# Kernel optimization log

Measured on AMD Instinct MI355X. Metric: run time of the kernel, lower is better.

The kernel has to match this reference:

```python
import jax, jax.numpy as jnp
import numpy as np
import math

C = 8  # sparsity factor c from __init__


def setup_inputs() -> dict:
    key = jax.random.key(0)
    kq, kk, kv, ki = jax.random.split(key, 4)
    B, Q, KV, D = 4, 2048, 2048, 512
    U = int(Q * math.log(KV))  # 15615 sampled keys, matches torch _sampler
    q = jax.random.normal(kq, (B, Q, D), dtype=jnp.float32)
    k = jax.random.normal(kk, (B, KV, D), dtype=jnp.float32)
    v = jax.random.normal(kv, (B, KV, D), dtype=jnp.float32)
    sample_idx = jax.random.randint(ki, (B, U), 0, KV)  # per-batch random key sample
    return {"q": q, "k": k, "v": v, "sample_idx": sample_idx}


def reference(q, k, v, sample_idx):
    B, Q, D = q.shape
    KV = k.shape[1]
    u = int(C * math.log(Q))  # number of selected queries (== 60 here)

    # _sampler: gather sampled keys per batch -> (B, U, D)
    k_bar = jnp.take_along_axis(k, sample_idx[:, :, None], axis=1)

    # sparsity measure M = max_j s_bar - mean_j s_bar, s_bar: (B, Q, U)
    s_bar = jnp.einsum('bqd,bud->bqu', q, k_bar)
    M = s_bar.max(axis=2) - s_bar.mean(axis=2)  # (B, Q)

    # top-u queries per batch
    _, top_idx = jax.lax.top_k(M, u)  # (B, u)
    q_bar = jnp.take_along_axis(q, top_idx[:, :, None], axis=1)  # (B, u, D)

    # small dense attention over full keys; NOTE: original scales by sqrt(kv_len)
    attn = jnp.einsum('bud,bkd->buk', q_bar, k) / jnp.sqrt(jnp.asarray(KV, q.dtype))
    attn = jax.nn.softmax(attn, axis=-1)
    s1 = jnp.einsum('buk,bkd->bud', attn, v)  # (B, u, D)

    # fill all positions with mean of v, then scatter attention outputs
    s = jnp.broadcast_to(v.mean(axis=1, keepdims=True), q.shape)  # (B, Q, D)
    bidx = jnp.arange(B)[:, None]
    s = s.at[bidx, top_idx].set(s1)
    return s
```

## Files before the change

kernel.cpp:

```cpp
#include <hip/hip_runtime.h>
#include <math.h>

#define BATCH 4
#define QN    2048
#define KVN   2048
#define DN    512
#define U_TOT 15615
#define NSEL  60
#define NSLOT 32
#define S1KS  64

typedef __attribute__((ext_vector_type(8))) short bf16x8;
typedef __attribute__((ext_vector_type(4))) float f32x4;

__device__ __forceinline__ unsigned short f2bf(float f) {
  unsigned u = __float_as_uint(f);
  unsigned r = (u + 0x7fffu + ((u >> 16) & 1u)) >> 16;
  return (unsigned short)r;
}
__device__ __forceinline__ float bf2f(unsigned short h) {
  return __uint_as_float(((unsigned)h) << 16);
}
__device__ __forceinline__ void gld16(const void* g, void* l) {
  __builtin_amdgcn_global_load_lds(
      (const __attribute__((address_space(1))) unsigned int*)g,
      (__attribute__((address_space(3))) unsigned int*)l, 16, 0, 0);
}

__global__ __launch_bounds__(256) void split_kernel(
    const float* __restrict__ q, const float* __restrict__ k,
    unsigned short* __restrict__ qhi, unsigned short* __restrict__ qlo,
    unsigned short* __restrict__ khi, unsigned short* __restrict__ klo)
{
  const int half = blockIdx.x >> 12;
  const int i = (blockIdx.x & 4095) * 256 + threadIdx.x;
  const float* in = half ? k : q;
  unsigned short* hi = half ? khi : qhi;
  unsigned short* lo = half ? klo : qlo;
  float4 f = reinterpret_cast<const float4*>(in)[i];
  ushort4 h, l;
  h.x = f2bf(f.x); l.x = f2bf(f.x - bf2f(h.x));
  h.y = f2bf(f.y); l.y = f2bf(f.y - bf2f(h.y));
  h.z = f2bf(f.z); l.z = f2bf(f.z - bf2f(h.z));
  h.w = f2bf(f.w); l.w = f2bf(f.w - bf2f(h.w));
  reinterpret_cast<ushort4*>(hi)[i] = h;
  reinterpret_cast<ushort4*>(lo)[i] = l;
}

__global__ __launch_bounds__(1024) void count_kernel(
    const int* __restrict__ sidx, float* __restrict__ cnt)
{
  __shared__ int h[KVN];
  const int b = blockIdx.x, t = threadIdx.x;
  for (int i = t; i < KVN; i += 1024) h[i] = 0;
  __syncthreads();
  for (int i = t; i < U_TOT; i += 1024) atomicAdd(&h[sidx[b * U_TOT + i]], 1);
  __syncthreads();
  for (int i = t; i < KVN; i += 1024) cnt[b * KVN + i] = (float)h[i];
}

__global__ __launch_bounds__(256) void s_mfma_kernel(
    const unsigned short* __restrict__ qh, const unsigned short* __restrict__ ql,
    const unsigned short* __restrict__ kh, const unsigned short* __restrict__ kl,
    const float* __restrict__ cnt, float* __restrict__ Pmax, float* __restrict__ Psum)
{
  __shared__ unsigned short Ah[128 * 32];
  __shared__ unsigned short Al[128 * 32];
  __shared__ unsigned short Bh[128 * 32];
  __shared__ unsigned short Bl[128 * 32];
  __shared__ float cnt_s[128];

  const int t = threadIdx.x;
  const int w = t >> 6;
  const int L = t & 63;
  const int mbase = (w & 1) * 64;
  const int nbase = (w >> 1) * 64;
  const int lm = L & 15;

  const int bid = blockIdx.x;
  const int xcd = bid & 7;
  const int idx = bid >> 3;
  const int b   = xcd >> 1;
  const int ji  = (xcd & 1) * 8 + (idx >> 3);
  const int qi0 = (idx & 7) * 2;
  const int j0  = ji * 128;

  if (t < 128) cnt_s[t] = cnt[b * KVN + j0 + t];

  const int srow = t >> 2;
  const int schk = (t & 3) ^ ((t >> 3) & 3);

  const int perm  = (L >> 4) ^ ((lm >> 1) & 3);
  const int abase = (mbase * 4 + lm * 4 + perm) * 8;
  const int bbase = (nbase * 4 + lm * 4 + perm) * 8;

  const size_t koff0 = ((size_t)(b * KVN) + j0 + srow) * DN + (size_t)(schk * 8);
  const size_t koff1 = koff0 + (size_t)64 * DN;

  for (int qq = 0; qq < 2; ++qq) {
    const int q0 = (qi0 + qq) * 128;
    const size_t qoff0 = ((size_t)(b * QN) + q0 + srow) * DN + (size_t)(schk * 8);
    const size_t qoff1 = qoff0 + (size_t)64 * DN;

    f32x4 acc[4][4];
#pragma unroll
    for (int nf = 0; nf < 4; ++nf)
#pragma unroll
      for (int mf = 0; mf < 4; ++mf) {
        acc[nf][mf][0] = 0.f; acc[nf][mf][1] = 0.f;
        acc[nf][mf][2] = 0.f; acc[nf][mf][3] = 0.f;
      }

    for (int d0 = 0; d0 < DN; d0 += 32) {
      __syncthreads();
      gld16(qh + qoff0 + d0, &Ah[t * 8]);
      gld16(qh + qoff1 + d0, &Ah[(t + 256) * 8]);
      gld16(ql + qoff0 + d0, &Al[t * 8]);
      gld16(ql + qoff1 + d0, &Al[(t + 256) * 8]);
      gld16(kh + koff0 + d0, &Bh[t * 8]);
      gld16(kh + koff1 + d0, &Bh[(t + 256) * 8]);
      gld16(kl + koff0 + d0, &Bl[t * 8]);
      gld16(kl + koff1 + d0, &Bl[(t + 256) * 8]);
      __syncthreads();

      bf16x8 ah[4], al[4];
#pragma unroll
      for (int mf = 0; mf < 4; ++mf) {
        ah[mf] = *reinterpret_cast<const bf16x8*>(&Ah[abase + mf * 512]);
        al[mf] = *reinterpret_cast<const bf16x8*>(&Al[abase + mf * 512]);
      }
#pragma unroll
      for (int nf = 0; nf < 4; ++nf) {
        bf16x8 bh = *reinterpret_cast<const bf16x8*>(&Bh[bbase + nf * 512]);
        bf16x8 bl = *reinterpret_cast<const bf16x8*>(&Bl[bbase + nf * 512]);
#pragma unroll
        for (int mf = 0; mf < 4; ++mf) {
          acc[nf][mf] = __builtin_amdgcn_mfma_f32_16x16x32_bf16(ah[mf], bh, acc[nf][mf], 0, 0, 0);
          acc[nf][mf] = __builtin_amdgcn_mfma_f32_16x16x32_bf16(ah[mf], bl, acc[nf][mf], 0, 0, 0);
          acc[nf][mf] = __builtin_amdgcn_mfma_f32_16x16x32_bf16(al[mf], bh, acc[nf][mf], 0, 0, 0);
        }
      }
    }

    float mx[4][4], wsm[4][4];
#pragma unroll
    for (int mf = 0; mf < 4; ++mf)
#pragma unroll
      for (int r = 0; r < 4; ++r) { mx[mf][r] = -INFINITY; wsm[mf][r] = 0.f; }

#pragma unroll
    for (int nf = 0; nf < 4; ++nf) {
      const float c = cnt_s[nbase + nf * 16 + lm];
      const bool has = (c > 0.f);
#pragma unroll
      for (int mf = 0; mf < 4; ++mf)
#pragma unroll
        for (int r = 0; r < 4; ++r) {
          const float v = acc[nf][mf][r];
          if (has) mx[mf][r] = fmaxf(mx[mf][r], v);
          wsm[mf][r] = fmaf(c, v, wsm[mf][r]);
        }
    }

    const size_t spi = (size_t)((ji * 2 + (w >> 1)) * BATCH + b);
#pragma unroll
    for (int mf = 0; mf < 4; ++mf)
#pragma unroll
      for (int r = 0; r < 4; ++r) {
        float m = mx[mf][r], s = wsm[mf][r];
#pragma unroll
        for (int o = 1; o < 16; o <<= 1) {
          m = fmaxf(m, __shfl_xor(m, o));
          s += __shfl_xor(s, o);
        }
        if (lm == 0) {
          const int qrow = q0 + mbase + mf * 16 + (L >> 4) * 4 + r;
          Pmax[spi * QN + qrow] = m;
          Psum[spi * QN + qrow] = s;
        }
      }
  }
}

__global__ __launch_bounds__(256) void combine_kernel(
    const float* __restrict__ Pmax, const float* __restrict__ Psum, float* __restrict__ M)
{
  const int g = blockIdx.x * 256 + threadIdx.x;
  const int b = g >> 11;
  const int qq = g & (QN - 1);
  float m = -INFINITY, s = 0.f;
#pragma unroll 4
  for (int p = 0; p < NSLOT; ++p) {
    m = fmaxf(m, Pmax[((size_t)(p * BATCH + b)) * QN + qq]);
    s += Psum[((size_t)(p * BATCH + b)) * QN + qq];
  }
  M[g] = m - s * (1.0f / (float)U_TOT);
}

__global__ __launch_bounds__(256) void select_kernel(
    const float* __restrict__ M, int* __restrict__ topidx, int* __restrict__ rowslot)
{
  const int b = blockIdx.x;
  const int t = threadIdx.x;
  unsigned long long key[8];
#pragma unroll
  for (int s = 0; s < 8; ++s) {
    const int qq = s * 256 + t;
    unsigned u = __float_as_uint(M[b * QN + qq]);
    u = (u & 0x80000000u) ? ~u : (u | 0x80000000u);
    key[s] = ((unsigned long long)u << 32) | (unsigned)(QN - qq);
    rowslot[b * QN + qq] = -1;
  }

  __shared__ unsigned hist[256];
  __shared__ unsigned long long pref_s;
  __shared__ unsigned rank_s;
  __shared__ unsigned cnt_s;
  if (t == 0) { pref_s = 0ull; rank_s = NSEL; cnt_s = 0u; }
  __syncthreads();

  for (int level = 7; level >= 0; --level) {
    const int shift = level * 8;
    hist[t] = 0;
    __syncthreads();
    const unsigned long long pref = pref_s;
    const unsigned rank = rank_s;
#pragma unroll
    for (int s = 0; s < 8; ++s) {
      const bool match = (level == 7) || ((key[s] >> (shift + 8)) == pref);
      if (match) atomicAdd(&hist[(unsigned)((key[s] >> shift) & 255u)], 1u);
    }
    __syncthreads();
    if (t < 64) {
      const unsigned h0 = hist[4 * t], h1 = hist[4 * t + 1];
      const unsigned h2 = hist[4 * t + 2], h3 = hist[4 * t + 3];
      const unsigned loc = h0 + h1 + h2 + h3;
      unsigned run = loc;
#pragma unroll
      for (int o = 1; o < 64; o <<= 1) {
        const unsigned oth = (unsigned)__shfl_down((int)run, o);
        if (t + o < 64) run += oth;
      }
      const unsigned suf = run - loc;
      const unsigned c3 = suf, c2 = c3 + h3, c1 = c2 + h2, c0 = c1 + h1;
      int hit = -1; unsigned cgt = 0;
      if      (c3 < rank && rank <= c3 + h3) { hit = 4 * t + 3; cgt = c3; }
      else if (c2 < rank && rank <= c2 + h2) { hit = 4 * t + 2; cgt = c2; }
      else if (c1 < rank && rank <= c1 + h1) { hit = 4 * t + 1; cgt = c1; }
      else if (c0 < rank && rank <= c0 + h0) { hit = 4 * t + 0; cgt = c0; }
      if (hit >= 0) {
        pref_s = ((level == 7) ? 0ull : (pref_s << 8)) | (unsigned long long)(unsigned)hit;
        rank_s = rank - cgt;
      }
    }
    __syncthreads();
  }

  const unsigned long long T = pref_s;
#pragma unroll
  for (int s = 0; s < 8; ++s) {
    if (key[s] >= T) {
      const unsigned pos = atomicAdd(&cnt_s, 1u);
      const int qsel = QN - (int)(key[s] & 0xFFFFFFFFull);
      topidx[b * 64 + pos] = qsel;
      rowslot[b * QN + qsel] = (int)pos;
    }
  }
}

#define SBM 64
#define SBN 32
#define SBK 32
__global__ __launch_bounds__(256) void scores_kernel(
    const float* __restrict__ q, const int* __restrict__ topidx,
    const float* __restrict__ k, float* __restrict__ attn)
{
  __shared__ float a_s[SBK][SBM + 4];
  __shared__ float b_s[SBK][SBN + 4];
  __shared__ int tix_s[64];
  const int t  = threadIdx.x;
  const int tx = t & 7;
  const int ty = t >> 3;
  const int kv0 = blockIdx.x * SBN;
  const int b   = blockIdx.y;
  const float* kb = k + (size_t)b * KVN * DN;

  if (t < 64) tix_s[t] = (t < NSEL) ? topidx[b * 64 + t] : 0;
  __syncthreads();

  float acc[2][4];
#pragma unroll
  for (int i = 0; i < 2; ++i)
#pragma unroll
    for (int j = 0; j < 4; ++j) acc[i][j] = 0.f;

  const int c4 = (t & 7) * 4;
  const int r0 = t >> 3;
  const int srow0 = tix_s[r0];
  const int srow1 = tix_s[r0 + 32];

  for (int d0 = 0; d0 < DN; d0 += SBK) {
#pragma unroll
    for (int rr = 0; rr < 2; ++rr) {
      int row = r0 + rr * 32;
      int srow = rr ? srow1 : srow0;
      float4 av = *reinterpret_cast<const float4*>(q + ((size_t)(b * QN) + srow) * DN + d0 + c4);
      a_s[c4 + 0][row] = av.x; a_s[c4 + 1][row] = av.y;
      a_s[c4 + 2][row] = av.z; a_s[c4 + 3][row] = av.w;
    }
    {
      float4 bv = *reinterpret_cast<const float4*>(kb + (size_t)(kv0 + r0) * DN + d0 + c4);
      b_s[c4 + 0][r0] = bv.x; b_s[c4 + 1][r0] = bv.y;
      b_s[c4 + 2][r0] = bv.z; b_s[c4 + 3][r0] = bv.w;
    }
    __syncthreads();
#pragma unroll
    for (int kk = 0; kk < SBK; ++kk) {
      const float a0 = a_s[kk][ty * 2];
      const float a1 = a_s[kk][ty * 2 + 1];
      float4 bv = *reinterpret_cast<const float4*>(&b_s[kk][tx * 4]);
      float bf[4] = {bv.x, bv.y, bv.z, bv.w};
#pragma unroll
      for (int j = 0; j < 4; ++j) {
        acc[0][j] = fmaf(a0, bf[j], acc[0][j]);
        acc[1][j] = fmaf(a1, bf[j], acc[1][j]);
      }
    }
    __syncthreads();
  }

#pragma unroll
  for (int i = 0; i < 2; ++i) {
    int j = ty * 2 + i;
    if (j < NSEL) {
      float4 o = make_float4(acc[i][0], acc[i][1], acc[i][2], acc[i][3]);
      *reinterpret_cast<float4*>(attn + ((size_t)(b * NSEL + j)) * KVN + kv0 + tx * 4) = o;
    }
  }
}

__global__ __launch_bounds__(256) void softmax_kernel(float* __restrict__ attn)
{
  __shared__ float buf[KVN];
  __shared__ float red[256];
  const int t = threadIdx.x;
  float* row = attn + (size_t)blockIdx.x * KVN;

  float m = -INFINITY;
  for (int i = t; i < KVN; i += 256) { float v = row[i]; buf[i] = v; m = fmaxf(m, v); }
  red[t] = m;
  __syncthreads();
  for (int off = 128; off > 0; off >>= 1) {
    if (t < off) red[t] = fmaxf(red[t], red[t + off]);
    __syncthreads();
  }
  m = red[0];
  __syncthreads();

  const float sc = 0.022097086912079608f;
  float s = 0.f;
  for (int i = t; i < KVN; i += 256) { float e = __expf((buf[i] - m) * sc); buf[i] = e; s += e; }
  red[t] = s;
  __syncthreads();
  for (int off = 128; off > 0; off >>= 1) {
    if (t < off) red[t] += red[t + off];
    __syncthreads();
  }
  float inv = 1.f / red[0];
  for (int i = t; i < KVN; i += 256) row[i] = buf[i] * inv;
}

__global__ __launch_bounds__(256) void s1_partial_kernel(
    const float* __restrict__ attn, const float* __restrict__ v,
    float* __restrict__ part, float* __restrict__ vpart)
{
  __shared__ float a_s[32][61];
  const int t    = threadIdx.x;
  const int dv4  = t & 63;
  const int jg   = t >> 6;
  const int dh   = blockIdx.x;
  const int b    = blockIdx.y;
  const int ks   = blockIdx.z;
  const int kv0  = ks * 32;
  const int dbase = dh * 256 + dv4 * 4;

  for (int x = t; x < NSEL * 32; x += 256) {
    const int j = x >> 5, kk = x & 31;
    a_s[kk][j] = attn[((size_t)(b * NSEL + j)) * KVN + kv0 + kk];
  }
  __syncthreads();

  f32x4 acc[15];
#pragma unroll
  for (int i = 0; i < 15; ++i) { acc[i][0] = 0.f; acc[i][1] = 0.f; acc[i][2] = 0.f; acc[i][3] = 0.f; }
  f32x4 vsum; vsum[0] = 0.f; vsum[1] = 0.f; vsum[2] = 0.f; vsum[3] = 0.f;

  const float* vb = v + ((size_t)b * KVN + kv0) * DN + dbase;
#pragma unroll 8
  for (int kk = 0; kk < 32; ++kk) {
    const f32x4 vv = *reinterpret_cast<const f32x4*>(vb + (size_t)kk * DN);
    if (jg == 0) { vsum[0] += vv[0]; vsum[1] += vv[1]; vsum[2] += vv[2]; vsum[3] += vv[3]; }
#pragma unroll
    for (int jj = 0; jj < 15; ++jj) {
      const float a = a_s[kk][jg * 15 + jj];
      acc[jj][0] = fmaf(a, vv[0], acc[jj][0]);
      acc[jj][1] = fmaf(a, vv[1], acc[jj][1]);
      acc[jj][2] = fmaf(a, vv[2], acc[jj][2]);
      acc[jj][3] = fmaf(a, vv[3], acc[jj][3]);
    }
  }

#pragma unroll
  for (int jj = 0; jj < 15; ++jj) {
    const int j = jg * 15 + jj;
    *reinterpret_cast<f32x4*>(
        part + ((size_t)((ks * BATCH + b) * NSEL) + j) * DN + dbase) = acc[jj];
  }
  if (jg == 0)
    *reinterpret_cast<f32x4*>(vpart + ((size_t)(ks * BATCH + b)) * DN + dbase) = vsum;
}

__global__ void vmean_combine_kernel(const float* __restrict__ vpart, float* __restrict__ vmean)
{
  int idx = blockIdx.x * 256 + threadIdx.x;
  if (idx < BATCH * DN) {
    int b = idx / DN, d = idx % DN;
    float s = 0.f;
    for (int c = 0; c < S1KS; ++c) s += vpart[(size_t)(c * BATCH + b) * DN + d];
    vmean[idx] = s * (1.0f / (float)KVN);
  }
}

__global__ __launch_bounds__(256) void out_kernel(
    const float* __restrict__ part, const float* __restrict__ vmean,
    const int* __restrict__ rowslot, float* __restrict__ out)
{
  const int gid = blockIdx.x * 256 + threadIdx.x;
  const int d4 = gid & 127;
  const int qq = (gid >> 7) & (QN - 1);
  const int b  = gid >> 18;
  const int slot = rowslot[b * QN + qq];
  f32x4 o;
  if (slot >= 0) {
    o[0] = 0.f; o[1] = 0.f; o[2] = 0.f; o[3] = 0.f;
    for (int ks = 0; ks < S1KS; ++ks) {
      const f32x4 p = reinterpret_cast<const f32x4*>(part)[
          ((size_t)((ks * BATCH + b) * NSEL) + slot) * (DN / 4) + d4];
      o[0] += p[0]; o[1] += p[1]; o[2] += p[2]; o[3] += p[3];
    }
  } else {
    o = reinterpret_cast<const f32x4*>(vmean)[b * (DN / 4) + d4];
  }
  reinterpret_cast<f32x4*>(out)[gid] = o;
}

extern "C" void kernel_launch(void* const* d_in, const int* in_sizes, int n_in,
                              void* d_out, int out_size, void* d_ws, size_t ws_size,
                              hipStream_t stream) {
  const float* q    = (const float*)d_in[0];
  const float* k    = (const float*)d_in[1];
  const float* v    = (const float*)d_in[2];
  const int*   sidx = (const int*)d_in[3];
  float* out = (float*)d_out;
  char*  W   = (char*)d_ws;

  const size_t NEL = (size_t)BATCH * QN * DN;
  unsigned short* qh = (unsigned short*)W;
  unsigned short* ql = qh + NEL;
  unsigned short* kh = ql + NEL;
  unsigned short* kl = kh + NEL;

  char* W2 = W + 37748736;
  float* cnt     = (float*)W2;
  float* Pmax    = (float*)(W2 + 32768);
  float* Psum    = (float*)(W2 + 32768 + 1048576);
  float* Mbuf    = (float*)(W2 + 32768 + 2097152);
  int*   topidx  = (int*)(W2 + 32768 + 2097152 + 32768);
  int*   rowslot = (int*)(W2 + 32768 + 2097152 + 32768 + 4096);

  float* attn  = (float*)W;
  float* part  = (float*)(W + 2097152);
  float* vpart = (float*)(W + 33554432);
  float* vmean = (float*)(W + 34078720);

  split_kernel<<<dim3(8192), 256, 0, stream>>>(q, k, qh, ql, kh, kl);
  count_kernel<<<dim3(BATCH), 1024, 0, stream>>>(sidx, cnt);
  s_mfma_kernel<<<dim3(512), 256, 0, stream>>>(qh, ql, kh, kl, cnt, Pmax, Psum);
  combine_kernel<<<dim3(BATCH * QN / 256), 256, 0, stream>>>(Pmax, Psum, Mbuf);
  select_kernel<<<dim3(BATCH), 256, 0, stream>>>(Mbuf, topidx, rowslot);
  scores_kernel<<<dim3(KVN / SBN, BATCH), 256, 0, stream>>>(q, topidx, k, attn);
  softmax_kernel<<<dim3(BATCH * NSEL), 256, 0, stream>>>(attn);
  s1_partial_kernel<<<dim3(2, BATCH, S1KS), 256, 0, stream>>>(attn, v, part, vpart);
  vmean_combine_kernel<<<dim3(8), 256, 0, stream>>>(vpart, vmean);
  out_kernel<<<dim3(4096), 256, 0, stream>>>(part, vmean, rowslot, out);
}
```

Baseline: 225.1 us.

## Restructure score GEMM into 256x256 double-buffered tiles with phased prefetch

The split-bf16 score GEMM moves from 128x128 tiles on 256 threads to 256x256 tiles on 512 threads (8 waves, 2 blocks per CU). The K loop now double-buffers LDS, interleaving global-to-LDS prefetch of the next slice with four MFMA phases separated by raw barriers, and raises wave priority around the MFMA bursts. The aim is to hide load latency and halve global reloads per output. The costs are more LDS (128KB per block) and more accumulator registers, which may limit occupancy, and only 256 blocks run.

Result: faster. 214.5 us (-4.7%).

```diff
diff --git a/kernel.cpp b/kernel.cpp
--- a/kernel.cpp
+++ b/kernel.cpp
@@ -59,126 +59,188 @@
   for (int i = t; i < KVN; i += 1024) cnt[b * KVN + i] = (float)h[i];
 }
 
-__global__ __launch_bounds__(256) void s_mfma_kernel(
+#define BAR() asm volatile("s_barrier" ::: "memory")
+
+#define PHASE_MFMA(P) \
+  __builtin_amdgcn_s_setprio(1); \
+  _Pragma("unroll") \
+  for (int n = 0; n < 4; ++n) { \
+    acc[2*(P)][n]   = __builtin_amdgcn_mfma_f32_16x16x32_bf16(a0h, bh_[n], acc[2*(P)][n], 0, 0, 0); \
+    acc[2*(P)][n]   = __builtin_amdgcn_mfma_f32_16x16x32_bf16(a0h, bl_[n], acc[2*(P)][n], 0, 0, 0); \
+    acc[2*(P)][n]   = __builtin_amdgcn_mfma_f32_16x16x32_bf16(a0l, bh_[n], acc[2*(P)][n], 0, 0, 0); \
+    acc[2*(P)+1][n] = __builtin_amdgcn_mfma_f32_16x16x32_bf16(a1h, bh_[n], acc[2*(P)+1][n], 0, 0, 0); \
+    acc[2*(P)+1][n] = __builtin_amdgcn_mfma_f32_16x16x32_bf16(a1h, bl_[n], acc[2*(P)+1][n], 0, 0, 0); \
+    acc[2*(P)+1][n] = __builtin_amdgcn_mfma_f32_16x16x32_bf16(a1l, bh_[n], acc[2*(P)+1][n], 0, 0, 0); \
+  } \
+  __builtin_amdgcn_s_setprio(0);
+
+#define LOAD_A(P, CB) \
+  a0h = *reinterpret_cast<const bf16x8*>(&Ah[CB][(4*(P)+wr)*512 + fr8]); \
+  a0l = *reinterpret_cast<const bf16x8*>(&Al[CB][(4*(P)+wr)*512 + fr8]); \
+  a1h = *reinterpret_cast<const bf16x8*>(&Ah[CB][(4*(P)+2+wr)*512 + fr8]); \
+  a1l = *reinterpret_cast<const bf16x8*>(&Al[CB][(4*(P)+2+wr)*512 + fr8]);
+
+#define LOAD_B(CB) \
+  _Pragma("unroll") \
+  for (int n = 0; n < 4; ++n) { \
+    bh_[n] = *reinterpret_cast<const bf16x8*>(&Bh[CB][wc*2048 + n*512 + fr8]); \
+    bl_[n] = *reinterpret_cast<const bf16x8*>(&Bl[CB][wc*2048 + n*512 + fr8]); \
+  }
+
+#define KSTEP_MAIN(CB, NB) { \
+  bf16x8 bh_[4], bl_[4], a0h, a0l, a1h, a1l; \
+  LOAD_B(CB) \
+  LOAD_A(0, CB) \
+  gld16(kh0, &Bh[NB][t*8]); gld16(kh1, &Bh[NB][4096 + t*8]); \
+  BAR(); \
+  PHASE_MFMA(0) \
+  BAR(); \
+  LOAD_A(1, CB) \
+  gld16(kl0, &Bl[NB][t*8]); gld16(kl1, &Bl[NB][4096 + t*8]); \
+  asm volatile("s_waitcnt vmcnt(4)" ::: "memory"); \
+  BAR(); \
+  PHASE_MFMA(1) \
+  BAR(); \
+  LOAD_A(2, CB) \
+  gld16(qh0, &Ah[NB][t*8]); gld16(ql0, &Al[NB][t*8]); \
+  BAR(); \
+  PHASE_MFMA(2) \
+  BAR(); \
+  LOAD_A(3, CB) \
+  gld16(qh1, &Ah[NB][4096 + t*8]); gld16(ql1, &Al[NB][4096 + t*8]); \
+  asm volatile("s_waitcnt vmcnt(2)" ::: "memory"); \
+  BAR(); \
+  PHASE_MFMA(3) \
+  BAR(); \
+  kh0 += 32; kh1 += 32; kl0 += 32; kl1 += 32; \
+  qh0 += 32; qh1 += 32; ql0 += 32; ql1 += 32; \
+}
+
+#define KSTEP_LAST(CB) { \
+  bf16x8 bh_[4], bl_[4], a0h, a0l, a1h, a1l; \
+  LOAD_B(CB) \
+  LOAD_A(0, CB) \
+  BAR(); \
+  PHASE_MFMA(0) \
+  BAR(); \
+  LOAD_A(1, CB) \
+  asm volatile("s_waitcnt vmcnt(0)" ::: "memory"); \
+  BAR(); \
+  PHASE_MFMA(1) \
+  BAR(); \
+  LOAD_A(2, CB) \
+  BAR(); \
+  PHASE_MFMA(2) \
+  BAR(); \
+  LOAD_A(3, CB) \
+  BAR(); \
+  PHASE_MFMA(3) \
+  BAR(); \
+}
+
+__global__ __launch_bounds__(512, 2) void s_mfma_kernel(
     const unsigned short* __restrict__ qh, const unsigned short* __restrict__ ql,
     const unsigned short* __restrict__ kh, const unsigned short* __restrict__ kl,
     const float* __restrict__ cnt, float* __restrict__ Pmax, float* __restrict__ Psum)
 {
-  __shared__ unsigned short Ah[128 * 32];
-  __shared__ unsigned short Al[128 * 32];
-  __shared__ unsigned short Bh[128 * 32];
-  __shared__ unsigned short Bl[128 * 32];
-  __shared__ float cnt_s[128];
+  __shared__ __align__(16) unsigned short Ah[2][8192];
+  __shared__ __align__(16) unsigned short Al[2][8192];
+  __shared__ __align__(16) unsigned short Bh[2][8192];
+  __shared__ __align__(16) unsigned short Bl[2][8192];
+  __shared__ float cnt_s[256];
 
   const int t = threadIdx.x;
   const int w = t >> 6;
   const int L = t & 63;
-  const int mbase = (w & 1) * 64;
-  const int nbase = (w >> 1) * 64;
   const int lm = L & 15;
+  const int wr = w >> 2;
+  const int wc = w & 3;
 
   const int bid = blockIdx.x;
   const int xcd = bid & 7;
   const int idx = bid >> 3;
   const int b   = xcd >> 1;
-  const int ji  = (xcd & 1) * 8 + (idx >> 3);
-  const int qi0 = (idx & 7) * 2;
-  const int j0  = ji * 128;
-
-  if (t < 128) cnt_s[t] = cnt[b * KVN + j0 + t];
+  const int ji  = (xcd & 1) * 4 + (idx >> 3);
+  const int qi  = idx & 7;
+  const int j0  = ji * 256;
+  const int q0  = qi * 256;
+
+  if (t < 256) cnt_s[t] = cnt[b * KVN + j0 + t];
 
   const int srow = t >> 2;
   const int schk = (t & 3) ^ ((t >> 3) & 3);
-
-  const int perm  = (L >> 4) ^ ((lm >> 1) & 3);
-  const int abase = (mbase * 4 + lm * 4 + perm) * 8;
-  const int bbase = (nbase * 4 + lm * 4 + perm) * 8;
-
-  const size_t koff0 = ((size_t)(b * KVN) + j0 + srow) * DN + (size_t)(schk * 8);
-  const size_t koff1 = koff0 + (size_t)64 * DN;
-
-  for (int qq = 0; qq < 2; ++qq) {
-    const int q0 = (qi0 + qq) * 128;
-    const size_t qoff0 = ((size_t)(b * QN) + q0 + srow) * DN + (size_t)(schk * 8);
-    const size_t qoff1 = qoff0 + (size_t)64 * DN;
-
-    f32x4 acc[4][4];
-#pragma unroll
-    for (int nf = 0; nf < 4; ++nf)
-#pragma unroll
-      for (int mf = 0; mf < 4; ++mf) {
-        acc[nf][mf][0] = 0.f; acc[nf][mf][1] = 0.f;
-        acc[nf][mf][2] = 0.f; acc[nf][mf][3] = 0.f;
+  const int perm = (L >> 4) ^ ((lm >> 1) & 3);
+  const int fr8  = (4 * lm + perm) * 8;
+
+  const size_t kof = ((size_t)(b * KVN) + j0 + srow) * DN + (size_t)(schk * 8);
+  const size_t qof = ((size_t)(b * QN) + q0 + srow) * DN + (size_t)(schk * 8);
+  const unsigned short* kh0 = kh + kof;
+  const unsigned short* kh1 = kh0 + (size_t)128 * DN;
+  const unsigned short* kl0 = kl + kof;
+  const unsigned short* kl1 = kl0 + (size_t)128 * DN;
+  const unsigned short* qh0 = qh + qof;
+  const unsigned short* qh1 = qh0 + (size_t)128 * DN;
+  const unsigned short* ql0 = ql + qof;
+  const unsigned short* ql1 = ql0 + (size_t)128 * DN;
+
+  f32x4 acc[8][4];
+#pragma unroll
+  for (int m = 0; m < 8; ++m)
+#pragma unroll
+    for (int n = 0; n < 4; ++n) {
+      acc[m][n][0] = 0.f; acc[m][n][1] = 0.f;
+      acc[m][n][2] = 0.f; acc[m][n][3] = 0.f;
+    }
+
+  gld16(kh0, &Bh[0][t*8]); gld16(kh1, &Bh[0][4096 + t*8]);
+  gld16(kl0, &Bl[0][t*8]); gld16(kl1, &Bl[0][4096 + t*8]);
+  gld16(qh0, &Ah[0][t*8]); gld16(ql0, &Al[0][t*8]);
+  gld16(qh1, &Ah[0][4096 + t*8]); gld16(ql1, &Al[0][4096 + t*8]);
+  kh0 += 32; kh1 += 32; kl0 += 32; kl1 += 32;
+  qh0 += 32; qh1 += 32; ql0 += 32; ql1 += 32;
+  asm volatile("s_waitcnt vmcnt(0) lgkmcnt(0)" ::: "memory");
+  BAR();
+
+#pragma unroll 1
+  for (int it = 0; it < 7; ++it) {
+    KSTEP_MAIN(0, 1)
+    KSTEP_MAIN(1, 0)
+  }
+  KSTEP_MAIN(0, 1)
+  KSTEP_LAST(1)
+
+  const int slot = ji * 4 + wc;
+  const size_t spi = (size_t)(slot * BATCH + b);
+  const int rgrp = (L >> 4) * 4;
+#pragma unroll
+  for (int m = 0; m < 8; ++m) {
+    float mx[4] = {-INFINITY, -INFINITY, -INFINITY, -INFINITY};
+    float ws[4] = {0.f, 0.f, 0.f, 0.f};
+#pragma unroll
+    for (int n = 0; n < 4; ++n) {
+      const float cw = cnt_s[wc * 64 + n * 16 + lm];
+      const bool has = (cw > 0.f);
+#pragma unroll
+      for (int r = 0; r < 4; ++r) {
+        const float v = acc[m][n][r];
+        if (has) mx[r] = fmaxf(mx[r], v);
+        ws[r] = fmaf(cw, v, ws[r]);
       }
-
-    for (int d0 = 0; d0 < DN; d0 += 32) {
-      __syncthreads();
-      gld16(qh + qoff0 + d0, &Ah[t * 8]);
-      gld16(qh + qoff1 + d0, &Ah[(t + 256) * 8]);
-      gld16(ql + qoff0 + d0, &Al[t * 8]);
-      gld16(ql + qoff1 + d0, &Al[(t + 256) * 8]);
-      gld16(kh + koff0 + d0, &Bh[t * 8]);
-      gld16(kh + koff1 + d0, &Bh[(t + 256) * 8]);
-      gld16(kl + koff0 + d0, &Bl[t * 8]);
-      gld16(kl + koff1 + d0, &Bl[(t + 256) * 8]);
-      __syncthreads();
-
-      bf16x8 ah[4], al[4];
-#pragma unroll
-      for (int mf = 0; mf < 4; ++mf) {
-        ah[mf] = *reinterpret_cast<const bf16x8*>(&Ah[abase + mf * 512]);
-        al[mf] = *reinterpret_cast<const bf16x8*>(&Al[abase + mf * 512]);
+    }
+#pragma unroll
+    for (int r = 0; r < 4; ++r) {
+      float mval = mx[r], sval = ws[r];
+#pragma unroll
+      for (int o = 1; o < 16; o <<= 1) {
+        mval = fmaxf(mval, __shfl_xor(mval, o));
+        sval += __shfl_xor(sval, o);
       }
-#pragma unroll
-      for (int nf = 0; nf < 4; ++nf) {
-        bf16x8 bh = *reinterpret_cast<const bf16x8*>(&Bh[bbase + nf * 512]);
-        bf16x8 bl = *reinterpret_cast<const bf16x8*>(&Bl[bbase + nf * 512]);
-#pragma unroll
-        for (int mf = 0; mf < 4; ++mf) {
-          acc[nf][mf] = __builtin_amdgcn_mfma_f32_16x16x32_bf16(ah[mf], bh, acc[nf][mf], 0, 0, 0);
-          acc[nf][mf] = __builtin_amdgcn_mfma_f32_16x16x32_bf16(ah[mf], bl, acc[nf][mf], 0, 0, 0);
-          acc[nf][mf] = __builtin_amdgcn_mfma_f32_16x16x32_bf16(al[mf], bh, acc[nf][mf], 0, 0, 0);
-        }
+      if (lm == 0) {
+        const int qrow = q0 + (2 * m + wr) * 16 + rgrp + r;
+        Pmax[spi * QN + qrow] = mval;
+        Psum[spi * QN + qrow] = sval;
       }
     }
-
-    float mx[4][4], wsm[4][4];
-#pragma unroll
-    for (int mf = 0; mf < 4; ++mf)
-#pragma unroll
-      for (int r = 0; r < 4; ++r) { mx[mf][r] = -INFINITY; wsm[mf][r] = 0.f; }
-
-#pragma unroll
-    for (int nf = 0; nf < 4; ++nf) {
-      const float c = cnt_s[nbase + nf * 16 + lm];
-      const bool has = (c > 0.f);
-#pragma unroll
-      for (int mf = 0; mf < 4; ++mf)
-#pragma unroll
-        for (int r = 0; r < 4; ++r) {
-          const float v = acc[nf][mf][r];
-          if (has) mx[mf][r] = fmaxf(mx[mf][r], v);
-          wsm[mf][r] = fmaf(c, v, wsm[mf][r]);
-        }
-    }
-
-    const size_t spi = (size_t)((ji * 2 + (w >> 1)) * BATCH + b);
-#pragma unroll
-    for (int mf = 0; mf < 4; ++mf)
-#pragma unroll
-      for (int r = 0; r < 4; ++r) {
-        float m = mx[mf][r], s = wsm[mf][r];
-#pragma unroll
-        for (int o = 1; o < 16; o <<= 1) {
-          m = fmaxf(m, __shfl_xor(m, o));
-          s += __shfl_xor(s, o);
-        }
-        if (lm == 0) {
-          const int qrow = q0 + mbase + mf * 16 + (L >> 4) * 4 + r;
-          Pmax[spi * QN + qrow] = m;
-          Psum[spi * QN + qrow] = s;
-        }
-      }
   }
 }
 
@@ -485,7 +547,7 @@
 
   split_kernel<<<dim3(8192), 256, 0, stream>>>(q, k, qh, ql, kh, kl);
   count_kernel<<<dim3(BATCH), 1024, 0, stream>>>(sidx, cnt);
-  s_mfma_kernel<<<dim3(512), 256, 0, stream>>>(qh, ql, kh, kl, cnt, Pmax, Psum);
+  s_mfma_kernel<<<dim3(256), 512, 0, stream>>>(qh, ql, kh, kl, cnt, Pmax, Psum);
   combine_kernel<<<dim3(BATCH * QN / 256), 256, 0, stream>>>(Pmax, Psum, Mbuf);
   select_kernel<<<dim3(BATCH), 256, 0, stream>>>(Mbuf, topidx, rowslot);
   scores_kernel<<<dim3(KVN / SBN, BATCH), 256, 0, stream>>>(q, topidx, k, attn);
```
